# Optimization experiments

Measured on AMD Instinct MI355X. Metric: run time of the kernel, lower is better.

The kernel has to match this reference:

```python
import jax, jax.numpy as jnp
import numpy as np

SEQ = 4096
E = 2048

def setup_inputs() -> dict:
    key = jax.random.key(0)
    kx, kq, kk, kv = jax.random.split(key, 4)
    scale = 1.0 / np.sqrt(E)
    x = jax.random.normal(kx, (SEQ, E), dtype=jnp.float32)
    # nn.Linear weights: shape [out, in], applied as x @ W.T
    Wq = jax.random.uniform(kq, (E, E), dtype=jnp.float32, minval=-scale, maxval=scale)
    Wk = jax.random.uniform(kk, (E, E), dtype=jnp.float32, minval=-scale, maxval=scale)
    Wv = jax.random.uniform(kv, (E, E), dtype=jnp.float32, minval=-scale, maxval=scale)
    return {"x": x, "Wq": Wq, "Wk": Wk, "Wv": Wv}

def reference(x, Wq, Wk, Wv):
    # q/k/v projections: nn.Linear(bias=False) -> x @ W.T
    q = x @ Wq.T  # [S, E]
    k = x @ Wk.T  # [S, E]
    v = x @ Wv.T  # [S, E]
    s = q @ k.T  # [S, S]
    w = jax.nn.softmax(s / jnp.sqrt(jnp.float32(E)), axis=-1)
    return w @ v  # [S, E]
```

## Files before the change

kernel.cpp:

```cpp
#include <hip/hip_runtime.h>
#include <hip/hip_bf16.h>

#define S_DIM 4096
#define E_DIM 2048

typedef __attribute__((ext_vector_type(4))) float f32x4;
typedef __attribute__((ext_vector_type(8))) short bf16x8;

__device__ __forceinline__ unsigned short f2bf(float f) {
  unsigned u = __builtin_bit_cast(unsigned, f);
  u += 0x7FFFu + ((u >> 16) & 1u);
  return (unsigned short)(u >> 16);
}
__device__ __forceinline__ float bf2f(unsigned short h) {
  return __builtin_bit_cast(float, ((unsigned)h) << 16);
}

__global__ __launch_bounds__(256) void cast_kernel(const float* __restrict__ in,
                                                   unsigned short* __restrict__ out,
                                                   int n4) {
  int i = blockIdx.x * 256 + threadIdx.x;
  if (i >= n4) return;
  float4 v = reinterpret_cast<const float4*>(in)[i];
  ushort4 o;
  o.x = f2bf(v.x); o.y = f2bf(v.y); o.z = f2bf(v.z); o.w = f2bf(v.w);
  reinterpret_cast<ushort4*>(out)[i] = o;
}

__global__ __launch_bounds__(256) void cast3_kernel(const float* __restrict__ w0,
                                                    const float* __restrict__ w1,
                                                    const float* __restrict__ w2,
                                                    unsigned short* __restrict__ out,
                                                    int n4each) {
  int i = blockIdx.x * 256 + threadIdx.x;
  if (i >= 3 * n4each) return;
  const float* src = (i < n4each) ? w0 : (i < 2 * n4each ? w1 : w2);
  int j = (i < n4each) ? i : (i < 2 * n4each ? i - n4each : i - 2 * n4each);
  float4 v = reinterpret_cast<const float4*>(src)[j];
  ushort4 o;
  o.x = f2bf(v.x); o.y = f2bf(v.y); o.z = f2bf(v.z); o.w = f2bf(v.w);
  reinterpret_cast<ushort4*>(out)[i] = o;
}

__global__ __launch_bounds__(256) void add_kernel(const float* __restrict__ a,
                                                  const float* __restrict__ b,
                                                  float* __restrict__ o, int n4) {
  int i = blockIdx.x * 256 + threadIdx.x;
  if (i >= n4) return;
  float4 va = reinterpret_cast<const float4*>(a)[i];
  float4 vb = reinterpret_cast<const float4*>(b)[i];
  float4 vo = {va.x + vb.x, va.y + vb.y, va.z + vb.z, va.w + vb.w};
  reinterpret_cast<float4*>(o)[i] = vo;
}


__device__ __forceinline__ void stage_half(const unsigned short* __restrict__ g,
                                           int grow0, int ld, int kByte0,
                                           char* ldsHalfBase, int tid) {
#pragma unroll
  for (int p = 0; p < 2; ++p) {
    const int o = (p * 512 + tid) * 16;
    const int S = o >> 10;
    const int oi = o & 1023;
    const int osi = oi ^ (((oi >> 9) & 1) << 5);
    const int r  = (S >> 1) * 16 + (osi >> 6);
    const int cb = (S & 1) * 64 + (osi & 63);
    const char* ga = reinterpret_cast<const char*>(g) +
                     ((size_t)(grow0 + r) * ld) * 2 + kByte0 + cb;
    char* la = ldsHalfBase + (o & ~1023);
    __builtin_amdgcn_global_load_lds(
        (const __attribute__((address_space(1))) void*)ga,
        (__attribute__((address_space(3))) void*)la, 16, 0, 0);
  }
}

#define MFMA_QUAD(AM, AN, AF, BF)                                              \
  _Pragma("unroll") for (int mm = 0; mm < 4; ++mm)                             \
  _Pragma("unroll") for (int nn = 0; nn < 2; ++nn)                             \
  _Pragma("unroll") for (int ks = 0; ks < 2; ++ks)                             \
    acc[(AM) + mm][(AN) + nn] = __builtin_amdgcn_mfma_f32_16x16x32_bf16(       \
        AF[mm][ks], BF[nn][ks], acc[(AM) + mm][(AN) + nn], 0, 0, 0);

#define READ_A0(dst, buf)                                                      \
  _Pragma("unroll") for (int mm = 0; mm < 4; ++mm)                             \
  _Pragma("unroll") for (int ks = 0; ks < 2; ++ks)                             \
    dst[mm][ks] = *reinterpret_cast<const bf16x8*>(                            \
        (buf) + aBase + (mm * 2 + ks) * 1024 + rsw);

#define READ_A1(dst, buf)                                                      \
  _Pragma("unroll") for (int mm = 0; mm < 4; ++mm)                             \
  _Pragma("unroll") for (int ks = 0; ks < 2; ++ks)                             \
    dst[mm][ks] = *reinterpret_cast<const bf16x8*>(                            \
        (buf) + aBase + ((4 + mm) * 2 + ks) * 1024 + rsw);

#define READ_B(dst, buf, nh)                                                   \
  _Pragma("unroll") for (int nn = 0; nn < 2; ++nn)                             \
  _Pragma("unroll") for (int ks = 0; ks < 2; ++ks)                             \
    dst[nn][ks] = *reinterpret_cast<const bf16x8*>(                            \
        (buf) + bSub[nh][nn] + ks * 1024 + rsw);

enum { EPI_QKV = 0, EPI_BF16 = 1, EPI_F32 = 2 };

template <int EPI>
__global__ __launch_bounds__(512, 2) void gemm8(
    const unsigned short* __restrict__ A, const unsigned short* __restrict__ B,
    int lda, int ldb, int K,
    float* __restrict__ Cf, unsigned short* __restrict__ Cb,
    unsigned short* __restrict__ Ct, int ldc, float scale,
    int kElemPerZ, long long zStrideC) {
  extern __shared__ char lds[];

  const int tid = threadIdx.x;
  const int rowA0 = blockIdx.y * 256;
  const int rowB0 = blockIdx.x * 256;
  const int k0B = blockIdx.z * kElemPerZ * 2;
  if (EPI == EPI_F32) Cf += (size_t)blockIdx.z * zStrideC;

  const int wave = tid >> 6;
  const int lane = tid & 63;
  const int wm = wave >> 2;
  const int wn = wave & 3;
  const int l15 = lane & 15;
  const int kg = lane >> 4;
  const int rsw = (l15 * 64 + kg * 16) ^ ((l15 & 8) << 2);

  int bSub[2][2];
#pragma unroll
  for (int nh = 0; nh < 2; ++nh)
#pragma unroll
    for (int nn = 0; nn < 2; ++nn) {
      const int row = wn * 64 + nh * 32 + nn * 16;
      bSub[nh][nn] = 32768 + (row >> 7) * 16384 + ((row & 127) >> 4) * 2048;
    }
  const int aBase = wm * 16384;

  f32x4 acc[8][4];
#pragma unroll
  for (int mi = 0; mi < 8; ++mi)
#pragma unroll
    for (int ni = 0; ni < 4; ++ni) acc[mi][ni] = (f32x4){0.f, 0.f, 0.f, 0.f};

  const int NT = K / 64;
  char* buf0 = lds;
  char* buf1 = lds + 65536;

  stage_half(A, rowA0,       lda, k0B,       buf0 + 0,     tid);
  stage_half(A, rowA0 + 128, lda, k0B,       buf0 + 16384, tid);
  stage_half(B, rowB0,       ldb, k0B,       buf0 + 32768, tid);
  stage_half(B, rowB0 + 128, ldb, k0B,       buf0 + 49152, tid);
  stage_half(A, rowA0,       lda, k0B + 128, buf1 + 0,     tid);
  stage_half(A, rowA0 + 128, lda, k0B + 128, buf1 + 16384, tid);
  stage_half(B, rowB0,       ldb, k0B + 128, buf1 + 32768, tid);
  stage_half(B, rowB0 + 128, ldb, k0B + 128, buf1 + 49152, tid);
  asm volatile("s_waitcnt vmcnt(8)" ::: "memory");
  __builtin_amdgcn_sched_barrier(0);
  __builtin_amdgcn_s_barrier();

  bf16x8 a0[4][2], a1[4][2], b0[2][2], b1[2][2];
  READ_A0(a0, buf0)
  READ_B(b0, buf0, 0)
  __builtin_amdgcn_sched_barrier(0);

  for (int t = 0; t < NT; ++t) {
    char* bufc = lds + (t & 1) * 65536;
    char* bufn = lds + ((t & 1) ^ 1) * 65536;

    READ_B(b1, bufc, 1)
    __builtin_amdgcn_s_barrier();
    asm volatile("s_waitcnt lgkmcnt(4)" ::: "memory");
    __builtin_amdgcn_sched_barrier(0);
    __builtin_amdgcn_s_setprio(1);
    MFMA_QUAD(0, 0, a0, b0)
    __builtin_amdgcn_s_setprio(0);
    __builtin_amdgcn_s_barrier();

    READ_A1(a1, bufc)
    __builtin_amdgcn_s_barrier();
    asm volatile("s_waitcnt lgkmcnt(8)" ::: "memory");
    __builtin_amdgcn_sched_barrier(0);
    __builtin_amdgcn_s_setprio(1);
    MFMA_QUAD(0, 2, a0, b1)
    __builtin_amdgcn_s_setprio(0);
    __builtin_amdgcn_s_barrier();

    if (t + 2 < NT) {
      const int kb = k0B + (t + 2) * 128;
      stage_half(B, rowB0,       ldb, kb, bufc + 32768, tid);
      stage_half(B, rowB0 + 128, ldb, kb, bufc + 49152, tid);
      asm volatile("s_waitcnt vmcnt(4)" ::: "memory");
    } else if (t + 1 < NT) {
      asm volatile("s_waitcnt vmcnt(0)" ::: "memory");
    }
    __builtin_amdgcn_sched_barrier(0);
    __builtin_amdgcn_s_barrier();
    asm volatile("s_waitcnt lgkmcnt(0)" ::: "memory");
    __builtin_amdgcn_sched_barrier(0);
    __builtin_amdgcn_s_setprio(1);
    MFMA_QUAD(4, 2, a1, b1)
    __builtin_amdgcn_s_setprio(0);
    __builtin_amdgcn_s_barrier();

    if (t + 1 < NT) { READ_A0(a0, bufn) }
    if (t + 2 < NT) {
      const int kb = k0B + (t + 2) * 128;
      stage_half(A, rowA0,       lda, kb, bufc + 0,     tid);
      stage_half(A, rowA0 + 128, lda, kb, bufc + 16384, tid);
    }
    __builtin_amdgcn_sched_barrier(0);
    __builtin_amdgcn_s_barrier();
    __builtin_amdgcn_s_setprio(1);
    MFMA_QUAD(4, 0, a1, b0)
    __builtin_amdgcn_s_setprio(0);
    __builtin_amdgcn_sched_barrier(0);
    if (t + 1 < NT) { READ_B(b0, bufn, 0) }
    __builtin_amdgcn_sched_barrier(0);
    __builtin_amdgcn_s_barrier();
  }

  const int r0 = rowA0 + wm * 128;
  const int c0 = rowB0 + wn * 64;
#pragma unroll
  for (int mi = 0; mi < 8; ++mi) {
    const int row = r0 + (mi >> 2) * 64 + (mi & 3) * 16 + kg * 4;
#pragma unroll
    for (int ni = 0; ni < 4; ++ni) {
      const int col = c0 + (ni >> 1) * 32 + (ni & 1) * 16 + l15;
      f32x4 v = acc[mi][ni];
      if constexpr (EPI == EPI_F32) {
#pragma unroll
        for (int r = 0; r < 4; ++r)
          Cf[(size_t)(row + r) * ldc + col] = v[r];
      } else if constexpr (EPI == EPI_BF16) {
#pragma unroll
        for (int r = 0; r < 4; ++r)
          Cb[(size_t)(row + r) * ldc + col] = f2bf(v[r] * scale);
      } else {
        if (rowB0 < 4096) {
#pragma unroll
          for (int r = 0; r < 4; ++r)
            Cb[(size_t)(row + r) * 4096 + col] = f2bf(v[r]);
        } else {
          ushort4 pk;
          pk.x = f2bf(v[0]); pk.y = f2bf(v[1]);
          pk.z = f2bf(v[2]); pk.w = f2bf(v[3]);
          *reinterpret_cast<ushort4*>(Ct + (size_t)(col - 4096) * 4096 + row) = pk;
        }
      }
    }
  }
}

__global__ __launch_bounds__(256) void softmax_kernel(const unsigned short* __restrict__ Sm,
                                                      unsigned short* __restrict__ P) {
  const int row = blockIdx.x;
  const int tid = threadIdx.x;
  const unsigned short* src = Sm + (size_t)row * S_DIM;
  float vals[16];
  float mx = -1e30f;
#pragma unroll
  for (int i = 0; i < 4; ++i) {
    ushort4 h = reinterpret_cast<const ushort4*>(src)[tid + i * 256];
    float a = bf2f(h.x), b = bf2f(h.y), c = bf2f(h.z), d = bf2f(h.w);
    vals[i * 4 + 0] = a; vals[i * 4 + 1] = b;
    vals[i * 4 + 2] = c; vals[i * 4 + 3] = d;
    mx = fmaxf(mx, fmaxf(fmaxf(a, b), fmaxf(c, d)));
  }
#pragma unroll
  for (int off = 32; off >= 1; off >>= 1) mx = fmaxf(mx, __shfl_xor(mx, off, 64));
  __shared__ float red[8];
  const int wave = tid >> 6, lane = tid & 63;
  if (lane == 0) red[wave] = mx;
  __syncthreads();
  mx = fmaxf(fmaxf(red[0], red[1]), fmaxf(red[2], red[3]));
  float sum = 0.f;
#pragma unroll
  for (int i = 0; i < 16; ++i) { vals[i] = __expf(vals[i] - mx); sum += vals[i]; }
#pragma unroll
  for (int off = 32; off >= 1; off >>= 1) sum += __shfl_xor(sum, off, 64);
  if (lane == 0) red[4 + wave] = sum;
  __syncthreads();
  sum = red[4] + red[5] + red[6] + red[7];
  const float inv = 1.0f / sum;
  unsigned short* dst = P + (size_t)row * S_DIM;
#pragma unroll
  for (int i = 0; i < 4; ++i) {
    ushort4 pk;
    pk.x = f2bf(vals[i * 4 + 0] * inv);
    pk.y = f2bf(vals[i * 4 + 1] * inv);
    pk.z = f2bf(vals[i * 4 + 2] * inv);
    pk.w = f2bf(vals[i * 4 + 3] * inv);
    reinterpret_cast<ushort4*>(dst)[tid + i * 256] = pk;
  }
}

extern "C" void kernel_launch(void* const* d_in, const int* in_sizes, int n_in,
                              void* d_out, int out_size, void* d_ws, size_t ws_size,
                              hipStream_t stream) {
  const float* x  = (const float*)d_in[0];
  const float* Wq = (const float*)d_in[1];
  const float* Wk = (const float*)d_in[2];
  const float* Wv = (const float*)d_in[3];
  float* out = (float*)d_out;
  char* ws = (char*)d_ws;

  const size_t MB = 1024 * 1024;
  const size_t NEED = 120 * MB;
  if (ws_size < NEED) return;

  unsigned short* xb   = (unsigned short*)(ws);
  unsigned short* wcat = (unsigned short*)(ws + 16 * MB);
  unsigned short* qkb  = (unsigned short*)(ws + 40 * MB);
  unsigned short* vt   = (unsigned short*)(ws + 72 * MB);
  unsigned short* Sb   = (unsigned short*)(ws + 88 * MB);
  float* outp0 = (float*)(ws);
  float* outp1 = (float*)(ws + 88 * MB);
  unsigned short* P = qkb;

  hipFuncSetAttribute(reinterpret_cast<const void*>(&gemm8<EPI_QKV>),
                      hipFuncAttributeMaxDynamicSharedMemorySize, 131072);
  hipFuncSetAttribute(reinterpret_cast<const void*>(&gemm8<EPI_BF16>),
                      hipFuncAttributeMaxDynamicSharedMemorySize, 131072);
  hipFuncSetAttribute(reinterpret_cast<const void*>(&gemm8<EPI_F32>),
                      hipFuncAttributeMaxDynamicSharedMemorySize, 131072);

  const int nx4 = S_DIM * E_DIM / 4;
  const int nw4 = E_DIM * E_DIM / 4;

  cast_kernel<<<nx4 / 256, 256, 0, stream>>>(x, xb, nx4);
  cast3_kernel<<<3 * nw4 / 256, 256, 0, stream>>>(Wq, Wk, Wv, wcat, nw4);

  gemm8<EPI_QKV><<<dim3(24, 16, 1), 512, 131072, stream>>>(
      xb, wcat, E_DIM, E_DIM, E_DIM, nullptr, qkb, vt, 4096, 1.0f, 0, 0);

  const float scale = 0.022097086912079608f;
  gemm8<EPI_BF16><<<dim3(16, 16, 1), 512, 131072, stream>>>(
      qkb, qkb + 2048, 4096, 4096, E_DIM, nullptr, Sb, nullptr, 4096, scale, 0, 0);

  softmax_kernel<<<S_DIM, 256, 0, stream>>>(Sb, P);

  gemm8<EPI_F32><<<dim3(8, 16, 2), 512, 131072, stream>>>(
      P, vt, 4096, 4096, 2048, outp0, nullptr, nullptr, E_DIM, 1.0f,
      2048, (long long)(88 * MB) / 4);

  add_kernel<<<nx4 / 256, 256, 0, stream>>>(outp0, outp1, out, nx4);
}
```

Before: 403.5 us.

## Restructure GEMM main loop into two MFMA phases with reordered staging

Rewrites the bf16 MFMA GEMM main loop from four quarter-phases with cross-iteration register prefetch into two half-phases per K tile. All B fragments and the first A half are read at the start of each iteration. The prefetch schedule changes so the second A half of the next tile is staged one iteration later, into the buffer just consumed. This cuts barriers and waitcnt points per iteration, but removes the overlap of LDS reads for the next tile with the current MFMAs and delays part of the global prefetch, which risks exposed latency.

```diff
diff --git a/kernel.cpp b/kernel.cpp
--- a/kernel.cpp
+++ b/kernel.cpp
@@ -74,12 +74,18 @@
   }
 }
 
-#define MFMA_QUAD(AM, AN, AF, BF)                                              \
-  _Pragma("unroll") for (int mm = 0; mm < 4; ++mm)                             \
-  _Pragma("unroll") for (int nn = 0; nn < 2; ++nn)                             \
+#define MFMA_HALF(AM, AF)                                                      \
   _Pragma("unroll") for (int ks = 0; ks < 2; ++ks)                             \
-    acc[(AM) + mm][(AN) + nn] = __builtin_amdgcn_mfma_f32_16x16x32_bf16(       \
-        AF[mm][ks], BF[nn][ks], acc[(AM) + mm][(AN) + nn], 0, 0, 0);
+  _Pragma("unroll") for (int mm = 0; mm < 4; ++mm) {                           \
+    acc[(AM) + mm][0] = __builtin_amdgcn_mfma_f32_16x16x32_bf16(               \
+        AF[mm][ks], b0[0][ks], acc[(AM) + mm][0], 0, 0, 0);                    \
+    acc[(AM) + mm][1] = __builtin_amdgcn_mfma_f32_16x16x32_bf16(               \
+        AF[mm][ks], b0[1][ks], acc[(AM) + mm][1], 0, 0, 0);                    \
+    acc[(AM) + mm][2] = __builtin_amdgcn_mfma_f32_16x16x32_bf16(               \
+        AF[mm][ks], b1[0][ks], acc[(AM) + mm][2], 0, 0, 0);                    \
+    acc[(AM) + mm][3] = __builtin_amdgcn_mfma_f32_16x16x32_bf16(               \
+        AF[mm][ks], b1[1][ks], acc[(AM) + mm][3], 0, 0, 0);                    \
+  }
 
 #define READ_A0(dst, buf)                                                      \
   _Pragma("unroll") for (int mm = 0; mm < 4; ++mm)                             \
@@ -144,51 +150,44 @@
   char* buf0 = lds;
   char* buf1 = lds + 65536;
 
+  stage_half(B, rowB0,       ldb, k0B,       buf0 + 32768, tid);
+  stage_half(B, rowB0 + 128, ldb, k0B,       buf0 + 49152, tid);
   stage_half(A, rowA0,       lda, k0B,       buf0 + 0,     tid);
   stage_half(A, rowA0 + 128, lda, k0B,       buf0 + 16384, tid);
-  stage_half(B, rowB0,       ldb, k0B,       buf0 + 32768, tid);
-  stage_half(B, rowB0 + 128, ldb, k0B,       buf0 + 49152, tid);
-  stage_half(A, rowA0,       lda, k0B + 128, buf1 + 0,     tid);
-  stage_half(A, rowA0 + 128, lda, k0B + 128, buf1 + 16384, tid);
   stage_half(B, rowB0,       ldb, k0B + 128, buf1 + 32768, tid);
   stage_half(B, rowB0 + 128, ldb, k0B + 128, buf1 + 49152, tid);
-  asm volatile("s_waitcnt vmcnt(8)" ::: "memory");
+  stage_half(A, rowA0,       lda, k0B + 128, buf1 + 0,     tid);
+  asm volatile("s_waitcnt vmcnt(6)" ::: "memory");
   __builtin_amdgcn_sched_barrier(0);
   __builtin_amdgcn_s_barrier();
-
-  bf16x8 a0[4][2], a1[4][2], b0[2][2], b1[2][2];
-  READ_A0(a0, buf0)
-  READ_B(b0, buf0, 0)
-  __builtin_amdgcn_sched_barrier(0);
 
   for (int t = 0; t < NT; ++t) {
     char* bufc = lds + (t & 1) * 65536;
     char* bufn = lds + ((t & 1) ^ 1) * 65536;
-
+    bf16x8 a0[4][2], a1[4][2], b0[2][2], b1[2][2];
+
+    READ_A0(a0, bufc)
+    READ_B(b0, bufc, 0)
     READ_B(b1, bufc, 1)
+    if (t + 1 < NT)
+      stage_half(A, rowA0 + 128, lda, k0B + (t + 1) * 128, bufn + 16384, tid);
+    __builtin_amdgcn_sched_barrier(0);
     __builtin_amdgcn_s_barrier();
-    asm volatile("s_waitcnt lgkmcnt(4)" ::: "memory");
+    asm volatile("s_waitcnt lgkmcnt(0)" ::: "memory");
     __builtin_amdgcn_sched_barrier(0);
     __builtin_amdgcn_s_setprio(1);
-    MFMA_QUAD(0, 0, a0, b0)
+    MFMA_HALF(0, a0)
     __builtin_amdgcn_s_setprio(0);
     __builtin_amdgcn_s_barrier();
 
     READ_A1(a1, bufc)
-    __builtin_amdgcn_s_barrier();
-    asm volatile("s_waitcnt lgkmcnt(8)" ::: "memory");
-    __builtin_amdgcn_sched_barrier(0);
-    __builtin_amdgcn_s_setprio(1);
-    MFMA_QUAD(0, 2, a0, b1)
-    __builtin_amdgcn_s_setprio(0);
-    __builtin_amdgcn_s_barrier();
-
     if (t + 2 < NT) {
       const int kb = k0B + (t + 2) * 128;
       stage_half(B, rowB0,       ldb, kb, bufc + 32768, tid);
       stage_half(B, rowB0 + 128, ldb, kb, bufc + 49152, tid);
-      asm volatile("s_waitcnt vmcnt(4)" ::: "memory");
-    } else if (t + 1 < NT) {
+      stage_half(A, rowA0,       lda, kb, bufc + 0,     tid);
+      asm volatile("s_waitcnt vmcnt(6)" ::: "memory");
+    } else {
       asm volatile("s_waitcnt vmcnt(0)" ::: "memory");
     }
     __builtin_amdgcn_sched_barrier(0);
@@ -196,24 +195,8 @@
     asm volatile("s_waitcnt lgkmcnt(0)" ::: "memory");
     __builtin_amdgcn_sched_barrier(0);
     __builtin_amdgcn_s_setprio(1);
-    MFMA_QUAD(4, 2, a1, b1)
+    MFMA_HALF(4, a1)
     __builtin_amdgcn_s_setprio(0);
-    __builtin_amdgcn_s_barrier();
-
-    if (t + 1 < NT) { READ_A0(a0, bufn) }
-    if (t + 2 < NT) {
-      const int kb = k0B + (t + 2) * 128;
-      stage_half(A, rowA0,       lda, kb, bufc + 0,     tid);
-      stage_half(A, rowA0 + 128, lda, kb, bufc + 16384, tid);
-    }
-    __builtin_amdgcn_sched_barrier(0);
-    __builtin_amdgcn_s_barrier();
-    __builtin_amdgcn_s_setprio(1);
-    MFMA_QUAD(4, 0, a1, b0)
-    __builtin_amdgcn_s_setprio(0);
-    __builtin_amdgcn_sched_barrier(0);
-    if (t + 1 < NT) { READ_B(b0, bufn, 0) }
-    __builtin_amdgcn_sched_barrier(0);
     __builtin_amdgcn_s_barrier();
   }
 
```

After: 398.1 us. No clear change (-1.3%).
